# Kernel optimization log

Measured on AMD Instinct MI355X. Metric: run time of the kernel, lower is better.

## Reference

```python
import jax, jax.numpy as jnp
import numpy as np

N_BITS = 6
N_STATES = 1 << N_BITS  # 64
BATCH = 262144
SINKHORN_ITERS = 50
EPS = 0.1
TINY = 1e-8


def hamming_cost(n_bits: int) -> jnp.ndarray:
    """(2^n, 2^n) Hamming distance between all binary states (== torch.cdist p=0)."""
    n = 1 << n_bits
    states = (np.arange(n)[:, None] >> np.arange(n_bits)[None, :]) & 1  # (n, n_bits)
    dist = (states[:, None, :] != states[None, :, :]).sum(-1)           # (n, n)
    return jnp.asarray(dist, dtype=jnp.float32)


def setup_inputs() -> dict:
    key = jax.random.key(0)
    k1, k2 = jax.random.split(key)
    p = jax.random.uniform(k1, (BATCH, N_STATES), dtype=jnp.float32)
    q = jax.random.uniform(k2, (BATCH, N_STATES), dtype=jnp.float32)
    cost_matrix = hamming_cost(N_BITS)  # registered buffer in the torch module
    return {"p": p, "q": q, "cost_matrix": cost_matrix}


def reference(p, q, cost_matrix):
    # normalize with the same epsilon smoothing as the torch module
    p = p + TINY
    q = q + TINY
    p = p / p.sum(axis=-1, keepdims=True)
    q = q / q.sum(axis=-1, keepdims=True)

    K = jnp.exp(-cost_matrix / EPS)  # (n, n)

    def step(carry, _):
        u, _v = carry
        # torch: (K.T @ u[...,None]).squeeze(-1)  ==  u @ K
        v = q / (u @ K)
        # torch: (K @ v[...,None]).squeeze(-1)    ==  v @ K.T
        u_new = p / (v @ K.T)
        return (u_new, v), None

    init = (jnp.ones_like(p), jnp.ones_like(q))
    (u, v), _ = jax.lax.scan(step, init, None, length=SINKHORN_ITERS)

    # emd_b = sum_ij u_bi * K_ij * v_bj * C_ij, without materializing (B,n,n)
    emd = jnp.einsum("bi,ij,bj->b", u, K * cost_matrix, v)
    return emd
```

## Files before the change

### kernel.cpp

```cpp
#include <hip/hip_runtime.h>


namespace {

typedef float v2f __attribute__((ext_vector_type(2)));

constexpr int   N     = 64;
constexpr int   NP    = 32;
constexpr int   NBITS = 6;
constexpr int   ITERS = 50;

constexpr double Ad = 4.5399929762484854e-05;
constexpr float  A  = (float)Ad;
constexpr float  EMD_SCALE = (float)(Ad / (1.0 - Ad * Ad));
constexpr float  EMD_DIAG  = (float)(6.0 * Ad * Ad / (1.0 - Ad * Ad));

__device__ __forceinline__ float rcp(float x) { return __builtin_amdgcn_rcpf(x); }

__device__ __forceinline__ void butterfly_pk(v2f W[NP], v2f A2) {
#pragma unroll
  for (int k = 0; k < NP; ++k) {
    v2f d;
    asm("v_pk_fma_f32 %0, %1, %2, %3 op_sel:[0,1,0] op_sel_hi:[1,0,1]"
        : "=v"(d) : "v"(A2), "v"(W[k]), "v"(W[k]));
    W[k] = d;
  }
#pragma unroll
  for (int b = 1; b < NBITS; ++b) {
    const int m = 1 << (b - 1);
#pragma unroll
    for (int k = 0; k < NP; ++k) {
      if ((k & m) == 0) {
        const int j = k | m;
        const v2f t0 = W[k], t1 = W[j];
        v2f d0, d1;
        asm("v_pk_fma_f32 %0, %1, %2, %3" : "=v"(d0) : "v"(A2), "v"(t1), "v"(t0));
        asm("v_pk_fma_f32 %0, %1, %2, %3" : "=v"(d1) : "v"(A2), "v"(t0), "v"(t1));
        W[k] = d0;
        W[j] = d1;
      }
    }
  }
}

__device__ __forceinline__ void div_step(v2f W[NP], const v2f X[NP]) {
#pragma unroll
  for (int k = 0; k < NP; ++k) {
    v2f rv;
    rv.x = rcp(W[k].x * W[k].y);
    v2f c, d;
    asm("v_pk_mul_f32 %0, %1, %2 op_sel:[0,1] op_sel_hi:[1,0]"
        : "=v"(c) : "v"(X[k]), "v"(W[k]));
    asm("v_pk_mul_f32 %0, %1, %2 op_sel:[0,0] op_sel_hi:[1,0]"
        : "=v"(d) : "v"(c), "v"(rv));
    W[k] = d;
  }
}

__global__ __launch_bounds__(256, 2) void emd_sinkhorn_kernel(
    const float* __restrict__ gp, const float* __restrict__ gq,
    float* __restrict__ out, int nbatch) {
  const int b = blockIdx.x * 256 + threadIdx.x;
  if (b >= nbatch) return;

  const float4* __restrict__ p4 =
      reinterpret_cast<const float4*>(gp) + (size_t)b * (N / 4);
  const float4* __restrict__ q4 =
      reinterpret_cast<const float4*>(gq) + (size_t)b * (N / 4);

  v2f P[NP], Q[NP], W[NP];

#pragma unroll
  for (int k = 0; k < N / 4; ++k) {
    const float4 tp = p4[k];
    P[2 * k + 0] = v2f{tp.x, tp.y};
    P[2 * k + 1] = v2f{tp.z, tp.w};
    const float4 tq = q4[k];
    Q[2 * k + 0] = v2f{tq.x, tq.y};
    Q[2 * k + 1] = v2f{tq.z, tq.w};
  }

  float sp0 = 0.f, sq0 = 0.f;
#pragma unroll
  for (int k = 0; k < NP; ++k) {
    sp0 += P[k].x + P[k].y;
    sq0 += Q[k].x + Q[k].y;
  }
  const float qscale = sp0 * rcp(sq0);
#pragma unroll
  for (int k = 0; k < NP; ++k) {
    Q[k].x *= qscale;
    Q[k].y *= qscale;
  }

#pragma unroll
  for (int k = 0; k < NP; ++k) {
    asm volatile("" : "+v"(P[k]));
    asm volatile("" : "+v"(Q[k]));
  }

  v2f A2 = v2f{A, A};
  asm volatile("" : "+v"(A2));

#pragma unroll
  for (int k = 0; k < NP; ++k) W[k] = Q[k];

#pragma unroll 1
  for (int it = 0; it < ITERS - 1; ++it) {
    butterfly_pk(W, A2);
    div_step(W, P);
    butterfly_pk(W, A2);
    div_step(W, Q);
  }

  butterfly_pk(W, A2);

  float ws[N];
#pragma unroll
  for (int k = 0; k < NP; ++k) {
    ws[2 * k + 0] = W[k].x;
    ws[2 * k + 1] = W[k].y;
  }

  float sp = 0.f;
  float sx = 0.f;
#pragma unroll
  for (int k = 0; k < NP; ++k) {
#pragma unroll
    for (int h = 0; h < 2; ++h) {
      const int i = 2 * k + h;
      const float pi = h ? P[k].y : P[k].x;
      sp += pi;
      const float ui = pi * rcp(ws[i]);
      float nb = ws[i ^ 1];
#pragma unroll
      for (int bb = 1; bb < NBITS; ++bb) nb += ws[i ^ (1 << bb)];
      sx = fmaf(ui, nb, sx);
    }
  }

  out[b] = fmaf(sx * rcp(sp), EMD_SCALE, -EMD_DIAG);
}

}

extern "C" void kernel_launch(void* const* d_in, const int* in_sizes, int n_in,
                              void* d_out, int out_size, void* d_ws, size_t ws_size,
                              hipStream_t stream) {
  const float* p = (const float*)d_in[0];
  const float* q = (const float*)d_in[1];
  float* out = (float*)d_out;

  const int nbatch = in_sizes[0] / N;
  const int block = 256;
  const int grid = (nbatch + block - 1) / block;
  emd_sinkhorn_kernel<<<grid, block, 0, stream>>>(p, q, out, nbatch);
}
```

Measured before the change: 391.0 us.

## Split each batch row across two lanes with DPP exchange for top butterfly bit

Each batch row is now handled by a pair of adjacent lanes, each holding 32 of the 64 states. The highest Hamming butterfly stage and the reductions exchange data between the pair through DPP xor-1 swizzles. This halves per-thread register state and doubles thread count, with launch bounds raised to 4 blocks per CU for higher occupancy. The cost is extra DPP moves and unpacked FMAs in the cross-lane stage, and half the lanes sit idle on the final store.

```diff
diff --git a/kernel.cpp b/kernel.cpp
--- a/kernel.cpp
+++ b/kernel.cpp
@@ -5,8 +5,8 @@
 
 typedef float v2f __attribute__((ext_vector_type(2)));
 
-constexpr int   N     = 64;
-constexpr int   NP    = 32;
+constexpr int   NL    = 32;
+constexpr int   NPL   = 16;
 constexpr int   NBITS = 6;
 constexpr int   ITERS = 50;
 
@@ -17,19 +17,24 @@
 
 __device__ __forceinline__ float rcp(float x) { return __builtin_amdgcn_rcpf(x); }
 
-__device__ __forceinline__ void butterfly_pk(v2f W[NP], v2f A2) {
+__device__ __forceinline__ float dpp_xor1(float x) {
+  return __int_as_float(
+      __builtin_amdgcn_update_dpp(0, __float_as_int(x), 0xB1, 0xF, 0xF, true));
+}
+
+__device__ __forceinline__ void butterfly_lane(v2f W[NPL], v2f A2) {
 #pragma unroll
-  for (int k = 0; k < NP; ++k) {
+  for (int k = 0; k < NPL; ++k) {
     v2f d;
     asm("v_pk_fma_f32 %0, %1, %2, %3 op_sel:[0,1,0] op_sel_hi:[1,0,1]"
         : "=v"(d) : "v"(A2), "v"(W[k]), "v"(W[k]));
     W[k] = d;
   }
 #pragma unroll
-  for (int b = 1; b < NBITS; ++b) {
+  for (int b = 1; b < NBITS - 1; ++b) {
     const int m = 1 << (b - 1);
 #pragma unroll
-    for (int k = 0; k < NP; ++k) {
+    for (int k = 0; k < NPL; ++k) {
       if ((k & m) == 0) {
         const int j = k | m;
         const v2f t0 = W[k], t1 = W[j];
@@ -41,11 +46,18 @@
       }
     }
   }
+#pragma unroll
+  for (int k = 0; k < NPL; ++k) {
+    const float px = dpp_xor1(W[k].x);
+    const float py = dpp_xor1(W[k].y);
+    W[k].x = fmaf(A2.x, px, W[k].x);
+    W[k].y = fmaf(A2.y, py, W[k].y);
+  }
 }
 
-__device__ __forceinline__ void div_step(v2f W[NP], const v2f X[NP]) {
+__device__ __forceinline__ void div_step(v2f W[NPL], const v2f X[NPL]) {
 #pragma unroll
-  for (int k = 0; k < NP; ++k) {
+  for (int k = 0; k < NPL; ++k) {
     v2f rv;
     rv.x = rcp(W[k].x * W[k].y);
     v2f c, d;
@@ -57,21 +69,21 @@
   }
 }
 
-__global__ __launch_bounds__(256, 2) void emd_sinkhorn_kernel(
+__global__ __launch_bounds__(256, 4) void emd_sinkhorn_kernel(
     const float* __restrict__ gp, const float* __restrict__ gq,
     float* __restrict__ out, int nbatch) {
-  const int b = blockIdx.x * 256 + threadIdx.x;
-  if (b >= nbatch) return;
+  const int t = blockIdx.x * 256 + threadIdx.x;
+  if (t >= 2 * nbatch) return;
 
   const float4* __restrict__ p4 =
-      reinterpret_cast<const float4*>(gp) + (size_t)b * (N / 4);
+      reinterpret_cast<const float4*>(gp) + (size_t)t * (NL / 4);
   const float4* __restrict__ q4 =
-      reinterpret_cast<const float4*>(gq) + (size_t)b * (N / 4);
+      reinterpret_cast<const float4*>(gq) + (size_t)t * (NL / 4);
 
-  v2f P[NP], Q[NP], W[NP];
+  v2f P[NPL], Q[NPL], W[NPL];
 
 #pragma unroll
-  for (int k = 0; k < N / 4; ++k) {
+  for (int k = 0; k < NL / 4; ++k) {
     const float4 tp = p4[k];
     P[2 * k + 0] = v2f{tp.x, tp.y};
     P[2 * k + 1] = v2f{tp.z, tp.w};
@@ -82,19 +94,21 @@
 
   float sp0 = 0.f, sq0 = 0.f;
 #pragma unroll
-  for (int k = 0; k < NP; ++k) {
+  for (int k = 0; k < NPL; ++k) {
     sp0 += P[k].x + P[k].y;
     sq0 += Q[k].x + Q[k].y;
   }
+  sp0 += dpp_xor1(sp0);
+  sq0 += dpp_xor1(sq0);
   const float qscale = sp0 * rcp(sq0);
 #pragma unroll
-  for (int k = 0; k < NP; ++k) {
+  for (int k = 0; k < NPL; ++k) {
     Q[k].x *= qscale;
     Q[k].y *= qscale;
   }
 
 #pragma unroll
-  for (int k = 0; k < NP; ++k) {
+  for (int k = 0; k < NPL; ++k) {
     asm volatile("" : "+v"(P[k]));
     asm volatile("" : "+v"(Q[k]));
   }
@@ -103,43 +117,42 @@
   asm volatile("" : "+v"(A2));
 
 #pragma unroll
-  for (int k = 0; k < NP; ++k) W[k] = Q[k];
+  for (int k = 0; k < NPL; ++k) W[k] = Q[k];
 
 #pragma unroll 1
   for (int it = 0; it < ITERS - 1; ++it) {
-    butterfly_pk(W, A2);
+    butterfly_lane(W, A2);
     div_step(W, P);
-    butterfly_pk(W, A2);
+    butterfly_lane(W, A2);
     div_step(W, Q);
   }
 
-  butterfly_pk(W, A2);
+  butterfly_lane(W, A2);
 
-  float ws[N];
-#pragma unroll
-  for (int k = 0; k < NP; ++k) {
-    ws[2 * k + 0] = W[k].x;
-    ws[2 * k + 1] = W[k].y;
-  }
-
-  float sp = 0.f;
+  const float sp = sp0;
   float sx = 0.f;
 #pragma unroll
-  for (int k = 0; k < NP; ++k) {
+  for (int k = 0; k < NPL; ++k) {
 #pragma unroll
     for (int h = 0; h < 2; ++h) {
-      const int i = 2 * k + h;
       const float pi = h ? P[k].y : P[k].x;
-      sp += pi;
-      const float ui = pi * rcp(ws[i]);
-      float nb = ws[i ^ 1];
+      const float wj = h ? W[k].y : W[k].x;
+      const float ui = pi * rcp(wj);
+      const int j = 2 * k + h;
+      float nb = h ? W[k].x : W[k].y;
 #pragma unroll
-      for (int bb = 1; bb < NBITS; ++bb) nb += ws[i ^ (1 << bb)];
+      for (int bb = 1; bb < NBITS - 1; ++bb) {
+        const int jn = j ^ (1 << bb);
+        nb += (jn & 1) ? W[jn >> 1].y : W[jn >> 1].x;
+      }
+      nb += dpp_xor1(wj);
       sx = fmaf(ui, nb, sx);
     }
   }
+  sx += dpp_xor1(sx);
 
-  out[b] = fmaf(sx * rcp(sp), EMD_SCALE, -EMD_DIAG);
+  if ((t & 1) == 0)
+    out[t >> 1] = fmaf(sx * rcp(sp), EMD_SCALE, -EMD_DIAG);
 }
 
 }
@@ -151,8 +164,9 @@
   const float* q = (const float*)d_in[1];
   float* out = (float*)d_out;
 
-  const int nbatch = in_sizes[0] / N;
+  const int nbatch = in_sizes[0] / 64;
+  const int nthreads = 2 * nbatch;
   const int block = 256;
-  const int grid = (nbatch + block - 1) / block;
+  const int grid = (nthreads + block - 1) / block;
   emd_sinkhorn_kernel<<<grid, block, 0, stream>>>(p, q, out, nbatch);
 }
```

Result: slower. 424.7 us (+8.6%).
